# Kernel tuning notes

Measured on AMD Instinct MI355X. Metric: run time of the kernel, lower is better.

## Reference

```python
import jax, jax.numpy as jnp
import numpy as np
from jax import lax

RATE = 2
KSIZE = 3
FUSE_K = 3
PAD = 1
SCALE = 10.0
ESCAPE_NAN = 1e-4
DN = ('NCHW', 'OIHW', 'NCHW')


def _patches(x, k, s, p):
    # x: [C,H,W] -> [L, C, k, k]  (matches torch pad + unfold(2).unfold(3) + permute)
    C = x.shape[0]
    pt = lax.conv_general_dilated_patches(
        x[None], (k, k), (s, s), [(p, p), (p, p)], dimension_numbers=DN)[0]
    oh, ow = pt.shape[1], pt.shape[2]
    # feature dim ordered (c, kh, kw)
    return pt.reshape(C, k, k, oh * ow).transpose(3, 0, 1, 2)


def setup_inputs() -> dict:
    key = jax.random.key(0)
    k1, k2 = jax.random.split(key)
    f = jax.random.normal(k1, (2, 128, 128, 128), dtype=jnp.float32)
    b = jax.random.normal(k2, (2, 128, 128, 128), dtype=jnp.float32)
    mask = jnp.zeros((1, 1, 128, 128), dtype=jnp.float32)
    return {"f": f, "b": b, "mask": mask}


def reference(f, b, mask):
    B, C, H, W = f.shape
    kernel = 2 * RATE  # 4
    # raw background patches (values for conv_transpose), per sample: [L, C, 4, 4]
    raw_w = jax.vmap(lambda bi: _patches(bi, kernel, RATE, PAD))(b)
    # nearest downsample by rate (torch nearest with scale 1/2 == strided slice)
    fd = f[:, :, ::RATE, ::RATE]
    bd = b[:, :, ::RATE, ::RATE]
    md = mask[:, :, ::RATE, ::RATE]
    fh, fw = fd.shape[2], fd.shape[3]
    bh, bw = bd.shape[2], bd.shape[3]
    L = bh * bw
    # matching (key) patches: [B, L, C, 3, 3]
    w = jax.vmap(lambda bi: _patches(bi, KSIZE, 1, PAD))(bd)
    # mask patches -> mm[l] = 1 where patch mean == 0 (valid background)
    m = _patches(md[0], KSIZE, 1, PAD)           # [L, 1, 3, 3]
    mm = (jnp.mean(m, axis=(1, 2, 3)) == 0.0).astype(f.dtype)[:, None, None]  # [L,1,1]

    fuse_w = jnp.eye(FUSE_K, dtype=f.dtype).reshape(1, 1, FUSE_K, FUSE_K)

    def fuse_conv(y):
        return lax.conv_general_dilated(y, fuse_w, (1, 1), [(1, 1), (1, 1)],
                                        dimension_numbers=DN)

    def one(xi, wi, rwi):
        # xi: [C,fh,fw], wi: [L,C,3,3], rwi: [L,C,4,4]
        norm = jnp.sqrt(jnp.sum(wi * wi, axis=(1, 2, 3), keepdims=True))
        wn = wi / jnp.maximum(norm, ESCAPE_NAN)
        # correlation scores (QK^T analogue): [1, L, fh, fw]
        yi = lax.conv_general_dilated(xi[None], wn, (1, 1), [(1, 1), (1, 1)],
                                      dimension_numbers=DN)
        # diagonal fuse convs, exactly mirroring the torch view/permute sequence
        yi = yi.reshape(1, 1, fh * fw, bh * bw)
        yi = fuse_conv(yi)
        yi = yi.reshape(fh, fw, bh, bw).transpose(1, 0, 3, 2).reshape(1, 1, fh * fw, bh * bw)
        yi = fuse_conv(yi)
        yi = yi.reshape(fw, fh, bw, bh).transpose(1, 0, 3, 2)  # [fh, fw, bh, bw]
        # faithful to the torch .view (plain contiguous reshape, no transpose)
        yi = yi.reshape(bh * bw, fh, fw)
        yi = yi * mm
        yi = jax.nn.softmax(yi * SCALE, axis=0) * mm
        # conv_transpose2d(yi, rwi, stride=rate, padding=1) / 4
        wt = jnp.flip(rwi, axis=(2, 3)).transpose(1, 0, 2, 3)  # [C, L, 4, 4]
        p = kernel - 1 - PAD  # 2
        out = lax.conv_general_dilated(yi[None], wt, (1, 1), [(p, p), (p, p)],
                                       lhs_dilation=(RATE, RATE),
                                       dimension_numbers=DN) / 4.0
        return out[0]  # [C, H, W]

    y = jax.vmap(one)(fd, w, raw_w)  # [B, C, H, W]
    return y
```

## Files before the change

### kernel.cpp

```cpp
#include <hip/hip_runtime.h>

#define CC 128
#define HH 128
#define WW 128
#define DH 64
#define DW 64
#define LTOT 4096
#define K0S 384
#define K2 2048
#define GK 4096
#define GKH 2048
#define SCALE_F 10.0f
#define IMG ((size_t)CC * HH * WW)
#define PSTR 4104

typedef __attribute__((ext_vector_type(8))) short short8;
typedef __attribute__((ext_vector_type(4))) float f32x4;

struct Prep4 { const float* src[4]; unsigned short* dst[4]; float* ssq[4]; int lo[4]; };
struct PtrN2 { const float* ssq[2]; float* invn[2]; float* mmv[2]; };
struct PtrR2 { const float* src[2]; unsigned short* dst[2]; };

__device__ __forceinline__ unsigned short f2bf(float x) {
    union { float f; unsigned u; } v; v.f = x;
    unsigned r = v.u + 0x7fffu + ((v.u >> 16) & 1u);
    return (unsigned short)(r >> 16);
}
__device__ __forceinline__ float bf2f(unsigned short b) {
    union { unsigned u; float f; } v; v.u = ((unsigned)b) << 16;
    return v.f;
}

__device__ __forceinline__ f32x4 ld4u(const float* p) {
    f32x4 r; __builtin_memcpy(&r, p, 16); return r;
}

#define GLDS16(g, l) __builtin_amdgcn_global_load_lds( \
    (const __attribute__((address_space(1))) void*)(g), \
    (__attribute__((address_space(3))) void*)(l), 16, 0, 0)

__global__ __launch_bounds__(128) void split_ds_kernel(Prep4 P) {
    __shared__ float partial[2];
    int z = blockIdx.z;
    const float* __restrict__ src = P.src[z];
    unsigned short* __restrict__ dst = P.dst[z];
    int lo_in_seg1 = P.lo[z];
    int n = blockIdx.x;
    int c = threadIdx.x;
    int ny = n >> 6, nx = n & 63;
    float v = src[((size_t)c * HH + 2 * ny) * WW + 2 * nx];
    unsigned short hi = f2bf(v);
    unsigned short lo = f2bf(v - bf2f(hi));
    unsigned short* drow = dst + (size_t)n * K0S;
    drow[c]       = hi;
    drow[128 + c] = lo_in_seg1 ? lo : hi;
    drow[256 + c] = lo_in_seg1 ? hi : lo;

    float* ssq = P.ssq[z];
    if (ssq) {
        float s2 = v * v;
#pragma unroll
        for (int o = 32; o; o >>= 1) s2 += __shfl_xor(s2, o);
        if ((threadIdx.x & 63) == 0) partial[threadIdx.x >> 6] = s2;
        __syncthreads();
        if (threadIdx.x == 0) ssq[n] = partial[0] + partial[1];
    }
}

__global__ __launch_bounds__(256) void im2col_rawt_kernel(PtrR2 P) {
    int z = blockIdx.z;
    const float* __restrict__ src = P.src[z];
    unsigned short* __restrict__ dst = P.dst[z];
    int idx = blockIdx.x * 256 + threadIdx.x;
    int p = idx & (LTOT - 1);
    int m = idx >> 12;
    int px = p & 63, py = p >> 6;
    int ke = m & 3, kd = (m >> 2) & 3, c = m >> 4;
    int yy = 2 * py - 1 + kd, xx = 2 * px - 1 + ke;
    float v = 0.f;
    if (yy >= 0 && yy < HH && xx >= 0 && xx < WW)
        v = src[((size_t)c * HH + yy) * WW + xx];
    dst[idx] = f2bf(v);
}

__global__ void norm_mm_kernel(PtrN2 P, const float* __restrict__ mask) {
    int z = blockIdx.z;
    const float* __restrict__ ssq = P.ssq[z];
    float* __restrict__ inv_norm = P.invn[z];
    float* __restrict__ mmv = P.mmv[z];
    int p = blockIdx.x * blockDim.x + threadIdx.x;
    int px = p & 63, py = p >> 6;
    float s = 0.f, ms = 0.f;
    for (int di = -1; di <= 1; ++di)
        for (int dj = -1; dj <= 1; ++dj) {
            int y = py + di, x = px + dj;
            if (y >= 0 && y < DH && x >= 0 && x < DW) {
                s += ssq[y * 64 + x];
                ms += mask[(size_t)(2 * y) * WW + 2 * x];
            }
        }
    float n = sqrtf(s);
    if (n < 1e-4f) n = 1e-4f;
    inv_norm[p] = 1.f / n;
    mmv[p] = (ms == 0.f) ? 1.f : 0.f;
}

__global__ __launch_bounds__(256) void gemm_mfma(
    const unsigned short* __restrict__ Aop, const unsigned short* __restrict__ Bop,
    float* __restrict__ C, int M, int N, int K)
{
    __shared__ short As[128 * 64];
    __shared__ short Bs[128 * 64];
    int tid = threadIdx.x;
    int wave = tid >> 6, lane = tid & 63;
    int wm = (wave >> 1) * 64;
    int wn = (wave & 1) * 64;
    int bm = blockIdx.y * 128, bn = blockIdx.x * 128;

    int rowS = wave * 32;
    int lrow8 = lane >> 3;
    int gchunk = ((lane & 7) ^ lrow8) * 8;

    f32x4 acc[4][4] = {};

    int quad = lane >> 4;
    int r16 = lane & 15;
    int pc0 = ((quad)     ^ (r16 & 7)) * 8;
    int pc1 = ((4 + quad) ^ (r16 & 7)) * 8;

    const unsigned short* ap0 = Aop + (size_t)(bm + rowS +  0 + lrow8) * K + gchunk;
    const unsigned short* ap1 = Aop + (size_t)(bm + rowS +  8 + lrow8) * K + gchunk;
    const unsigned short* ap2 = Aop + (size_t)(bm + rowS + 16 + lrow8) * K + gchunk;
    const unsigned short* ap3 = Aop + (size_t)(bm + rowS + 24 + lrow8) * K + gchunk;
    const unsigned short* bp0 = Bop + (size_t)(bn + rowS +  0 + lrow8) * K + gchunk;
    const unsigned short* bp1 = Bop + (size_t)(bn + rowS +  8 + lrow8) * K + gchunk;
    const unsigned short* bp2 = Bop + (size_t)(bn + rowS + 16 + lrow8) * K + gchunk;
    const unsigned short* bp3 = Bop + (size_t)(bn + rowS + 24 + lrow8) * K + gchunk;
    short* lA = As + rowS * 64;
    short* lB = Bs + rowS * 64;

    for (int k0 = 0; k0 < K; k0 += 64) {
        GLDS16(ap0, lA);            GLDS16(ap1, lA + 8 * 64);
        GLDS16(ap2, lA + 16 * 64);  GLDS16(ap3, lA + 24 * 64);
        GLDS16(bp0, lB);            GLDS16(bp1, lB + 8 * 64);
        GLDS16(bp2, lB + 16 * 64);  GLDS16(bp3, lB + 24 * 64);
        ap0 += 64; ap1 += 64; ap2 += 64; ap3 += 64;
        bp0 += 64; bp1 += 64; bp2 += 64; bp3 += 64;
        __syncthreads();

        short8 a0[4], b0[4], a1[4], b1[4];
#pragma unroll
        for (int i = 0; i < 4; ++i) {
            a0[i] = *(const short8*)&As[(wm + i * 16 + r16) * 64 + pc0];
            b0[i] = *(const short8*)&Bs[(wn + i * 16 + r16) * 64 + pc0];
            a1[i] = *(const short8*)&As[(wm + i * 16 + r16) * 64 + pc1];
            b1[i] = *(const short8*)&Bs[(wn + i * 16 + r16) * 64 + pc1];
        }
#pragma unroll
        for (int i = 0; i < 4; ++i)
#pragma unroll
            for (int j = 0; j < 4; ++j) {
                acc[i][j] = __builtin_amdgcn_mfma_f32_16x16x32_bf16(a0[i], b0[j], acc[i][j], 0, 0, 0);
                acc[i][j] = __builtin_amdgcn_mfma_f32_16x16x32_bf16(a1[i], b1[j], acc[i][j], 0, 0, 0);
            }
        __syncthreads();
    }

    int col = lane & 15, rq = (lane >> 4) * 4;
#pragma unroll
    for (int i = 0; i < 4; ++i) {
#pragma unroll
        for (int r = 0; r < 4; ++r) {
            int m = bm + wm + i * 16 + rq + r;
#pragma unroll
            for (int j = 0; j < 4; ++j)
                C[(size_t)m * N + bn + wn + j * 16 + col] = acc[i][j][r];
        }
    }
}

__global__ __launch_bounds__(512, 2) void gemm_k2(
    const unsigned short* __restrict__ Aop, const unsigned short* __restrict__ Bop,
    float* __restrict__ Cpart)
{
    constexpr int NT = 32;
    constexpr int BUFS = 512 * 64;
    __shared__ short lds[2 * BUFS];
    int tid = threadIdx.x;
    int wave = tid >> 6, lane = tid & 63;
    int wm = (wave >> 2) * 128;
    int wn = (wave & 3) * 64;
    int bm = blockIdx.y * 256, bn = blockIdx.x * 256;
    int ks = blockIdx.z;
    int lrow8 = lane >> 3;
    int gchunk = ((lane & 7) ^ lrow8) * 8;
    int r16 = lane & 15, quad = lane >> 4;
    int pc0 = ((quad)     ^ (r16 & 7)) * 8;
    int pc1 = ((4 + quad) ^ (r16 & 7)) * 8;

    const size_t ko = (size_t)ks * GKH + gchunk;
    const unsigned short* ap0 = Aop + (size_t)(bm + wave * 32 +  0 + lrow8) * GK + ko;
    const unsigned short* ap1 = Aop + (size_t)(bm + wave * 32 +  8 + lrow8) * GK + ko;
    const unsigned short* ap2 = Aop + (size_t)(bm + wave * 32 + 16 + lrow8) * GK + ko;
    const unsigned short* ap3 = Aop + (size_t)(bm + wave * 32 + 24 + lrow8) * GK + ko;
    const unsigned short* bp0 = Bop + (size_t)(bn + wave * 32 +  0 + lrow8) * GK + ko;
    const unsigned short* bp1 = Bop + (size_t)(bn + wave * 32 +  8 + lrow8) * GK + ko;
    const unsigned short* bp2 = Bop + (size_t)(bn + wave * 32 + 16 + lrow8) * GK + ko;
    const unsigned short* bp3 = Bop + (size_t)(bn + wave * 32 + 24 + lrow8) * GK + ko;

    f32x4 acc[8][4] = {};

#define STAGE2(s) do { \
    short* la = lds + (s) * BUFS + (wave * 32) * 64; \
    short* lb = lds + (s) * BUFS + 256 * 64 + (wave * 32) * 64; \
    GLDS16(ap0, la);            GLDS16(ap1, la + 8 * 64); \
    GLDS16(ap2, la + 16 * 64);  GLDS16(ap3, la + 24 * 64); \
    GLDS16(bp0, lb);            GLDS16(bp1, lb + 8 * 64); \
    GLDS16(bp2, lb + 16 * 64);  GLDS16(bp3, lb + 24 * 64); \
    ap0 += 64; ap1 += 64; ap2 += 64; ap3 += 64; \
    bp0 += 64; bp1 += 64; bp2 += 64; bp3 += 64; } while (0)

    STAGE2(0); STAGE2(1);
    asm volatile("s_waitcnt vmcnt(8)" ::: "memory");
    __builtin_amdgcn_s_barrier();
    asm volatile("" ::: "memory");

    int buf = 0;
#pragma unroll 1
    for (int T = 0; T < NT; ++T) {
        const short* Ab = lds + buf * BUFS;
        const short* Bb = Ab + 256 * 64;
        short8 a0[8], a1[8], b0[4], b1[4];
#pragma unroll
        for (int j = 0; j < 4; ++j) {
            b0[j] = *(const short8*)&Bb[(wn + j * 16 + r16) * 64 + pc0];
            b1[j] = *(const short8*)&Bb[(wn + j * 16 + r16) * 64 + pc1];
        }
        a0[0] = *(const short8*)&Ab[(wm + r16) * 64 + pc0];
        a1[0] = *(const short8*)&Ab[(wm + r16) * 64 + pc1];
#pragma unroll
        for (int i = 0; i < 8; ++i) {
            if (i < 7) {
                a0[i + 1] = *(const short8*)&Ab[(wm + (i + 1) * 16 + r16) * 64 + pc0];
                a1[i + 1] = *(const short8*)&Ab[(wm + (i + 1) * 16 + r16) * 64 + pc1];
                asm volatile("s_waitcnt lgkmcnt(2)" ::: "memory");
            } else {
                asm volatile("s_waitcnt lgkmcnt(0)" ::: "memory");
            }
            __builtin_amdgcn_sched_barrier(0);
            __builtin_amdgcn_s_setprio(1);
#pragma unroll
            for (int j = 0; j < 4; ++j) {
                acc[i][j] = __builtin_amdgcn_mfma_f32_16x16x32_bf16(a0[i], b0[j], acc[i][j], 0, 0, 0);
                acc[i][j] = __builtin_amdgcn_mfma_f32_16x16x32_bf16(a1[i], b1[j], acc[i][j], 0, 0, 0);
            }
            __builtin_amdgcn_s_setprio(0);
        }
        asm volatile("s_waitcnt vmcnt(0)" ::: "memory");
        __builtin_amdgcn_s_barrier();
        asm volatile("" ::: "memory");
        if (T + 2 < NT) STAGE2(buf);
        buf ^= 1;
    }
#undef STAGE2

    float* Cout = Cpart + (size_t)ks * K2 * LTOT;
    int col = lane & 15, rq = (lane >> 4) * 4;
#pragma unroll
    for (int i = 0; i < 8; ++i) {
#pragma unroll
        for (int r = 0; r < 4; ++r) {
            int m = bm + wm + i * 16 + rq + r;
#pragma unroll
            for (int j = 0; j < 4; ++j)
                Cout[(size_t)m * LTOT + bn + wn + j * 16 + col] = acc[i][j][r];
        }
    }
}

__global__ __launch_bounds__(256) void stencil_norm_kernel(
    const float* __restrict__ C, const float* __restrict__ invn,
    float* __restrict__ Sg)
{
    int blk = blockIdx.x;
    int q = ((blk & 7) << 9) | (blk >> 3);
    int t = threadIdx.x;
    int qy = q >> 6, qx = q & 63;
    int chunk = t >> 2;
    int lanebase = (t & 3) << 4;
    int p0 = t << 4;

    f32x4 acc[4];
#pragma unroll
    for (int g = 0; g < 4; ++g) { acc[g][0] = acc[g][1] = acc[g][2] = acc[g][3] = 0.f; }

#pragma unroll
    for (int du = -1; du <= 1; ++du) {
        if (qy + du < 0 || qy + du > 63) continue;
        if (chunk + du < 0 || chunk + du > 63) continue;
#pragma unroll
        for (int dv = -1; dv <= 1; ++dv) {
            if (qx + dv < 0 || qx + dv > 63) continue;
            const float* rowp = C + (size_t)(q + 64 * du + dv) * LTOT + 64 * du + dv + p0;
#pragma unroll
            for (int g = 0; g < 4; ++g) {
                f32x4 lv = ld4u(rowp + 4 * g);
                if (dv == -1 && g == 0 && lanebase == 0)  lv[0] = 0.f;
                if (dv ==  1 && g == 3 && lanebase == 48) lv[3] = 0.f;
                acc[g] += lv;
            }
        }
    }
    float* orow = Sg + (size_t)q * PSTR;
#pragma unroll
    for (int g = 0; g < 4; ++g) {
        f32x4 iv = *(const f32x4*)(invn + p0 + 4 * g);
        *(f32x4*)(orow + p0 + 4 * g) = acc[g] * iv;
    }
    if (t == 0) { orow[-4] = orow[-3] = orow[-2] = orow[-1] = 0.f; }
    else if (t == 1) { orow[4096] = orow[4097] = orow[4098] = orow[4099] = 0.f; }
    if (q == 0) {
        float* gr = Sg - 4 - PSTR;
        for (int k = t; k < PSTR; k += 256) gr[k] = 0.f;
    }
    if (q == 4095) {
        float* gr = Sg - 4 + (size_t)4096 * PSTR;
        for (int k = t; k < PSTR; k += 256) gr[k] = 0.f;
    }
}

__global__ __launch_bounds__(256) void fused_conv_softmax_kernel(
    const float* __restrict__ Sg, const float* __restrict__ mmv,
    unsigned short* __restrict__ S16)
{
    __shared__ float redmax[4];
    __shared__ float redsum[4];
    int blk = blockIdx.x;
    int q = ((blk & 7) << 9) | (blk >> 3);
    int t = threadIdx.x;
    int lane = t & 63, wid = t >> 6;
    int chunk = t >> 2;
    int lanebase = (t & 3) << 4;
    int c0 = t << 4;

    int rbase = ((q & 63) << 6) | (q >> 6);

    f32x4 sacc[4];
#pragma unroll
    for (int g = 0; g < 4; ++g) { sacc[g][0] = sacc[g][1] = sacc[g][2] = sacc[g][3] = 0.f; }

#pragma unroll
    for (int j = 0; j < 3; ++j) {
        int r2 = rbase + (j - 1);
        if (r2 < 0 || r2 >= LTOT) continue;
        int rr = ((r2 & 63) << 6) | (r2 >> 6);
        int cj = chunk + (j - 1);
        int ccb;
        if (cj < 0)       ccb = 4031 + lanebase;
        else if (cj > 63) ccb = lanebase + 1;
        else              ccb = (cj << 6) + lanebase;
        const float* pr = Sg + (size_t)rr * PSTR + ccb;
#pragma unroll
        for (int g = 0; g < 4; ++g) {
            const float* pg = pr + 4 * g;
            f32x4 lm = ld4u(pg - (PSTR + 1));
            f32x4 l0 = ld4u(pg);
            f32x4 lp = ld4u(pg + (PSTR + 1));
            f32x4 tj = lm + l0 + lp;
            if (j == 0 && g == 0 && t == 0)   tj[0] = 0.f;
            if (j == 2 && g == 3 && t == 255) tj[3] = 0.f;
            sacc[g] += tj;
        }
    }

    float v[16];
#pragma unroll
    for (int g = 0; g < 4; ++g) {
        f32x4 m4 = *(const f32x4*)(mmv + c0 + 4 * g);
#pragma unroll
        for (int e = 0; e < 4; ++e)
            v[4 * g + e] = sacc[g][e] * m4[e] * SCALE_F;
    }
#pragma unroll
    for (int k = 0; k < 16; ++k) asm volatile("" : "+v"(v[k]));

    float mx = v[0];
#pragma unroll
    for (int i = 1; i < 16; ++i) mx = fmaxf(mx, v[i]);
#pragma unroll
    for (int o = 32; o; o >>= 1) mx = fmaxf(mx, __shfl_xor(mx, o));
    if (lane == 0) redmax[wid] = mx;
    __syncthreads();
    float gmx = fmaxf(fmaxf(redmax[0], redmax[1]), fmaxf(redmax[2], redmax[3]));

    float s = 0.f;
#pragma unroll
    for (int i = 0; i < 16; ++i) {
        v[i] = __expf(v[i] - gmx);
        s += v[i];
    }
#pragma unroll
    for (int o = 32; o; o >>= 1) s += __shfl_xor(s, o);
    if (lane == 0) redsum[wid] = s;
    __syncthreads();
    float inv = 1.f / (redsum[0] + redsum[1] + redsum[2] + redsum[3]);

    unsigned short* orow = S16 + (size_t)q * LTOT + c0;
    short8 h0, h1;
#pragma unroll
    for (int e = 0; e < 8; ++e) {
        h0[e] = (short)f2bf(v[e]     * inv * mmv[c0 + e]);
        h1[e] = (short)f2bf(v[8 + e] * inv * mmv[c0 + 8 + e]);
    }
    *(short8*)orow = h0;
    *(short8*)(orow + 8) = h1;
}

__global__ void output_kernel(const float* __restrict__ C2t, float* __restrict__ out) {
    const float* __restrict__ P1 = C2t + (size_t)K2 * LTOT;
    int idx = blockIdx.x * blockDim.x + threadIdx.x;
    int x = idx & 127;
    int y = (idx >> 7) & 127;
    int c = idx >> 14;
    int oylo = max(0, (y - 1) >> 1), oyhi = min(63, (y + 1) >> 1);
    int oxlo = max(0, (x - 1) >> 1), oxhi = min(63, (x + 1) >> 1);
    float s = 0.f;
    for (int oy = oylo; oy <= oyhi; ++oy)
        for (int ox = oxlo; ox <= oxhi; ++ox) {
            int kd = y - 2 * oy + 1;
            int ke = x - 2 * ox + 1;
            size_t off = (size_t)(c * 16 + kd * 4 + ke) * LTOT + oy * 64 + ox;
            s += C2t[off] + P1[off];
        }
    out[idx] = s * 0.25f;
}

extern "C" void kernel_launch(void* const* d_in, const int* in_sizes, int n_in,
                              void* d_out, int out_size, void* d_ws, size_t ws_size,
                              hipStream_t stream) {
    (void)in_sizes; (void)n_in; (void)out_size; (void)ws_size;
    const float* f    = (const float*)d_in[0];
    const float* b    = (const float*)d_in[1];
    const float* mask = (const float*)d_in[2];
    float* out = (float*)d_out;

    const size_t SZ_MAT  = (size_t)LTOT * LTOT * 4;
    const size_t SZ_SPAD = (size_t)PSTR * 4098 * 4;
    const size_t SZ_WR   = (size_t)K2 * LTOT * 2;
    const size_t SZ_SP   = (size_t)LTOT * K0S * 2;
    const size_t SZ_V    = (size_t)LTOT * 4;

    auto pad = [](size_t n) { return (n + 255) & ~(size_t)255; };
    char* p = (char*)d_ws;
    auto take = [&](size_t n) -> void* { void* r = (void*)p; p += pad(n); return r; };

    take(256);
    float* Buf1 = (float*)take(SZ_MAT);
    float* Spad = (float*)take(SZ_SPAD);
    unsigned short* W = (unsigned short*)take(SZ_WR);
    unsigned short* Bsp0 = (unsigned short*)take(SZ_SP);
    unsigned short* Fsp0 = (unsigned short*)take(SZ_SP);
    unsigned short* Bsp1 = (unsigned short*)take(SZ_SP);
    unsigned short* Fsp1 = (unsigned short*)take(SZ_SP);
    float* ssq0 = (float*)take(SZ_V);  float* ssq1 = (float*)take(SZ_V);
    float* invn0 = (float*)take(SZ_V); float* invn1 = (float*)take(SZ_V);
    float* mmv0 = (float*)take(SZ_V);  float* mmv1 = (float*)take(SZ_V);

    const float* f0 = f,  *b0 = b;
    const float* f1 = f + IMG, *b1 = b + IMG;

    float* Sg = Spad + PSTR + 4;
    unsigned short* S16 = (unsigned short*)Buf1;
    float* C2t = Spad;

    Prep4 P{{b0, f0, b1, f1}, {Bsp0, Fsp0, Bsp1, Fsp1},
            {ssq0, nullptr, ssq1, nullptr}, {1, 0, 1, 0}};
    split_ds_kernel<<<dim3(LTOT, 1, 4), 128, 0, stream>>>(P);
    PtrN2 nm{{ssq0, ssq1}, {invn0, invn1}, {mmv0, mmv1}};
    norm_mm_kernel<<<dim3(16, 1, 2), 256, 0, stream>>>(nm, mask);

    for (int bi = 0; bi < 2; ++bi) {
        const unsigned short* Fsp = bi ? Fsp1 : Fsp0;
        const unsigned short* Bsp = bi ? Bsp1 : Bsp0;
        const float* invn = bi ? invn1 : invn0;
        const float* mmv  = bi ? mmv1 : mmv0;

        PtrR2 rw{{bi ? b1 : b0, nullptr}, {W, nullptr}};
        im2col_rawt_kernel<<<dim3((size_t)K2 * LTOT / 256, 1, 1), 256, 0, stream>>>(rw);

        gemm_mfma<<<dim3(32, 32), 256, 0, stream>>>(Fsp, Bsp, Buf1, LTOT, LTOT, K0S);

        stencil_norm_kernel<<<LTOT, 256, 0, stream>>>(Buf1, invn, Sg);

        fused_conv_softmax_kernel<<<LTOT, 256, 0, stream>>>(Sg, mmv, S16);

        gemm_k2<<<dim3(LTOT / 256, K2 / 256, 2), 512, 0, stream>>>(W, S16, C2t);

        output_kernel<<<CC * HH * WW / 256, 256, 0, stream>>>(C2t, out + (size_t)bi * IMG);
    }
}
```

Before: 512.4 us.

## Restructure split-K GEMM main loop into four barrier-separated quadrant phases

```diff
diff --git a/kernel.cpp b/kernel.cpp
--- a/kernel.cpp
+++ b/kernel.cpp
@@ -184,8 +184,7 @@
     float* __restrict__ Cpart)
 {
     constexpr int NT = 32;
-    constexpr int BUFS = 512 * 64;
-    __shared__ short lds[2 * BUFS];
+    __shared__ short lds[65536];
     int tid = threadIdx.x;
     int wave = tid >> 6, lane = tid & 63;
     int wm = (wave >> 2) * 128;
@@ -197,72 +196,135 @@
     int r16 = lane & 15, quad = lane >> 4;
     int pc0 = ((quad)     ^ (r16 & 7)) * 8;
     int pc1 = ((4 + quad) ^ (r16 & 7)) * 8;
+    int ha = wave >> 2;
+    int hb = (wave & 3) >> 1;
 
     const size_t ko = (size_t)ks * GKH + gchunk;
-    const unsigned short* ap0 = Aop + (size_t)(bm + wave * 32 +  0 + lrow8) * GK + ko;
-    const unsigned short* ap1 = Aop + (size_t)(bm + wave * 32 +  8 + lrow8) * GK + ko;
-    const unsigned short* ap2 = Aop + (size_t)(bm + wave * 32 + 16 + lrow8) * GK + ko;
-    const unsigned short* ap3 = Aop + (size_t)(bm + wave * 32 + 24 + lrow8) * GK + ko;
-    const unsigned short* bp0 = Bop + (size_t)(bn + wave * 32 +  0 + lrow8) * GK + ko;
-    const unsigned short* bp1 = Bop + (size_t)(bn + wave * 32 +  8 + lrow8) * GK + ko;
-    const unsigned short* bp2 = Bop + (size_t)(bn + wave * 32 + 16 + lrow8) * GK + ko;
-    const unsigned short* bp3 = Bop + (size_t)(bn + wave * 32 + 24 + lrow8) * GK + ko;
+    const unsigned short* aS00 = Aop + (size_t)(bm +       wave * 16 +     lrow8) * GK + ko;
+    const unsigned short* aS01 = Aop + (size_t)(bm +       wave * 16 + 8 + lrow8) * GK + ko;
+    const unsigned short* aS10 = Aop + (size_t)(bm + 128 + wave * 16 +     lrow8) * GK + ko;
+    const unsigned short* aS11 = Aop + (size_t)(bm + 128 + wave * 16 + 8 + lrow8) * GK + ko;
+    const unsigned short* bS00 = Bop + (size_t)(bn +       wave * 16 +     lrow8) * GK + ko;
+    const unsigned short* bS01 = Bop + (size_t)(bn +       wave * 16 + 8 + lrow8) * GK + ko;
+    const unsigned short* bS10 = Bop + (size_t)(bn + 128 + wave * 16 +     lrow8) * GK + ko;
+    const unsigned short* bS11 = Bop + (size_t)(bn + 128 + wave * 16 + 8 + lrow8) * GK + ko;
+
+    const short* ArdH = lds + ha * 8192;
+    const short* BrdH = lds + 32768 + hb * 8192 + (wn & 64) * 64;
+    short* AstH = lds + (wave * 16) * 64;
+    short* BstH = lds + 32768 + (wave * 16) * 64;
 
     f32x4 acc[8][4] = {};
-
-#define STAGE2(s) do { \
-    short* la = lds + (s) * BUFS + (wave * 32) * 64; \
-    short* lb = lds + (s) * BUFS + 256 * 64 + (wave * 32) * 64; \
-    GLDS16(ap0, la);            GLDS16(ap1, la + 8 * 64); \
-    GLDS16(ap2, la + 16 * 64);  GLDS16(ap3, la + 24 * 64); \
-    GLDS16(bp0, lb);            GLDS16(bp1, lb + 8 * 64); \
-    GLDS16(bp2, lb + 16 * 64);  GLDS16(bp3, lb + 24 * 64); \
-    ap0 += 64; ap1 += 64; ap2 += 64; ap3 += 64; \
-    bp0 += 64; bp1 += 64; bp2 += 64; bp3 += 64; } while (0)
-
-    STAGE2(0); STAGE2(1);
+    short8 aa0[4], aa1[4], b0[4], b1[4];
+
+#define STAGE_B2(d) do { short* p = BstH + (d) * 16384; \
+    GLDS16(bS00, p);        GLDS16(bS01, p + 512); \
+    GLDS16(bS10, p + 8192); GLDS16(bS11, p + 8192 + 512); \
+    bS00 += 64; bS01 += 64; bS10 += 64; bS11 += 64; } while (0)
+#define STAGE_A2(d) do { short* p = AstH + (d) * 16384; \
+    GLDS16(aS00, p);        GLDS16(aS01, p + 512); \
+    GLDS16(aS10, p + 8192); GLDS16(aS11, p + 8192 + 512); \
+    aS00 += 64; aS01 += 64; aS10 += 64; aS11 += 64; } while (0)
+#define BARRIER do { __builtin_amdgcn_s_barrier(); asm volatile("" ::: "memory"); } while (0)
+#define WAIT_LGKM0 do { asm volatile("s_waitcnt lgkmcnt(0)" ::: "memory"); \
+    __builtin_amdgcn_sched_barrier(0); } while (0)
+#define MFMA_BF16 __builtin_amdgcn_mfma_f32_16x16x32_bf16
+
+    STAGE_B2(0); STAGE_A2(0); STAGE_B2(1); STAGE_A2(1);
     asm volatile("s_waitcnt vmcnt(8)" ::: "memory");
-    __builtin_amdgcn_s_barrier();
-    asm volatile("" ::: "memory");
-
-    int buf = 0;
+    BARRIER;
+    {
+        const short* Bb = BrdH;
+        b0[0] = *(const short8*)&Bb[(r16) * 64 + pc0];
+        b1[0] = *(const short8*)&Bb[(r16) * 64 + pc1];
+        b0[1] = *(const short8*)&Bb[(16 + r16) * 64 + pc0];
+        b1[1] = *(const short8*)&Bb[(16 + r16) * 64 + pc1];
+    }
+
 #pragma unroll 1
-    for (int T = 0; T < NT; ++T) {
-        const short* Ab = lds + buf * BUFS;
-        const short* Bb = Ab + 256 * 64;
-        short8 a0[8], a1[8], b0[4], b1[4];
-#pragma unroll
-        for (int j = 0; j < 4; ++j) {
-            b0[j] = *(const short8*)&Bb[(wn + j * 16 + r16) * 64 + pc0];
-            b1[j] = *(const short8*)&Bb[(wn + j * 16 + r16) * 64 + pc1];
-        }
-        a0[0] = *(const short8*)&Ab[(wm + r16) * 64 + pc0];
-        a1[0] = *(const short8*)&Ab[(wm + r16) * 64 + pc1];
-#pragma unroll
-        for (int i = 0; i < 8; ++i) {
-            if (i < 7) {
-                a0[i + 1] = *(const short8*)&Ab[(wm + (i + 1) * 16 + r16) * 64 + pc0];
-                a1[i + 1] = *(const short8*)&Ab[(wm + (i + 1) * 16 + r16) * 64 + pc1];
-                asm volatile("s_waitcnt lgkmcnt(2)" ::: "memory");
-            } else {
-                asm volatile("s_waitcnt lgkmcnt(0)" ::: "memory");
-            }
-            __builtin_amdgcn_sched_barrier(0);
-            __builtin_amdgcn_s_setprio(1);
-#pragma unroll
-            for (int j = 0; j < 4; ++j) {
-                acc[i][j] = __builtin_amdgcn_mfma_f32_16x16x32_bf16(a0[i], b0[j], acc[i][j], 0, 0, 0);
-                acc[i][j] = __builtin_amdgcn_mfma_f32_16x16x32_bf16(a1[i], b1[j], acc[i][j], 0, 0, 0);
-            }
-            __builtin_amdgcn_s_setprio(0);
-        }
-        asm volatile("s_waitcnt vmcnt(0)" ::: "memory");
-        __builtin_amdgcn_s_barrier();
-        asm volatile("" ::: "memory");
-        if (T + 2 < NT) STAGE2(buf);
-        buf ^= 1;
-    }
-#undef STAGE2
+    for (int t = 0; t < NT; ++t) {
+        int d = t & 1;
+        const short* Ab = ArdH + d * 16384;
+        const short* Bb = BrdH + d * 16384;
+
+#pragma unroll
+        for (int ii = 0; ii < 4; ++ii) {
+            aa0[ii] = *(const short8*)&Ab[(ii * 16 + r16) * 64 + pc0];
+            aa1[ii] = *(const short8*)&Ab[(ii * 16 + r16) * 64 + pc1];
+        }
+        BARRIER; WAIT_LGKM0;
+        __builtin_amdgcn_s_setprio(1);
+#pragma unroll
+        for (int ii = 0; ii < 4; ++ii)
+#pragma unroll
+            for (int j = 0; j < 2; ++j) {
+                acc[ii][j] = MFMA_BF16(aa0[ii], b0[j], acc[ii][j], 0, 0, 0);
+                acc[ii][j] = MFMA_BF16(aa1[ii], b1[j], acc[ii][j], 0, 0, 0);
+            }
+        __builtin_amdgcn_s_setprio(0);
+        BARRIER;
+
+        b0[2] = *(const short8*)&Bb[(32 + r16) * 64 + pc0];
+        b1[2] = *(const short8*)&Bb[(32 + r16) * 64 + pc1];
+        b0[3] = *(const short8*)&Bb[(48 + r16) * 64 + pc0];
+        b1[3] = *(const short8*)&Bb[(48 + r16) * 64 + pc1];
+        BARRIER; WAIT_LGKM0;
+        __builtin_amdgcn_s_setprio(1);
+#pragma unroll
+        for (int ii = 0; ii < 4; ++ii)
+#pragma unroll
+            for (int j = 2; j < 4; ++j) {
+                acc[ii][j] = MFMA_BF16(aa0[ii], b0[j], acc[ii][j], 0, 0, 0);
+                acc[ii][j] = MFMA_BF16(aa1[ii], b1[j], acc[ii][j], 0, 0, 0);
+            }
+        __builtin_amdgcn_s_setprio(0);
+        BARRIER;
+
+#pragma unroll
+        for (int ii = 0; ii < 4; ++ii) {
+            aa0[ii] = *(const short8*)&Ab[(64 + ii * 16 + r16) * 64 + pc0];
+            aa1[ii] = *(const short8*)&Ab[(64 + ii * 16 + r16) * 64 + pc1];
+        }
+        if (t + 2 < NT) STAGE_B2(d);
+        BARRIER; WAIT_LGKM0;
+        __builtin_amdgcn_s_setprio(1);
+#pragma unroll
+        for (int ii = 0; ii < 4; ++ii)
+#pragma unroll
+            for (int j = 0; j < 2; ++j) {
+                acc[4 + ii][j] = MFMA_BF16(aa0[ii], b0[j], acc[4 + ii][j], 0, 0, 0);
+                acc[4 + ii][j] = MFMA_BF16(aa1[ii], b1[j], acc[4 + ii][j], 0, 0, 0);
+            }
+        __builtin_amdgcn_s_setprio(0);
+        BARRIER;
+
+        if (t + 2 < NT) { asm volatile("s_waitcnt vmcnt(4)" ::: "memory"); }
+        else            { asm volatile("s_waitcnt vmcnt(0)" ::: "memory"); }
+        if (t + 1 < NT) {
+            const short* Bn = BrdH + (d ^ 1) * 16384;
+            b0[0] = *(const short8*)&Bn[(r16) * 64 + pc0];
+            b1[0] = *(const short8*)&Bn[(r16) * 64 + pc1];
+            b0[1] = *(const short8*)&Bn[(16 + r16) * 64 + pc0];
+            b1[1] = *(const short8*)&Bn[(16 + r16) * 64 + pc1];
+        }
+        if (t + 2 < NT) STAGE_A2(d);
+        BARRIER; WAIT_LGKM0;
+        __builtin_amdgcn_s_setprio(1);
+#pragma unroll
+        for (int ii = 0; ii < 4; ++ii)
+#pragma unroll
+            for (int j = 2; j < 4; ++j) {
+                acc[4 + ii][j] = MFMA_BF16(aa0[ii], b0[j], acc[4 + ii][j], 0, 0, 0);
+                acc[4 + ii][j] = MFMA_BF16(aa1[ii], b1[j], acc[4 + ii][j], 0, 0, 0);
+            }
+        __builtin_amdgcn_s_setprio(0);
+        BARRIER;
+    }
+#undef STAGE_B2
+#undef STAGE_A2
+#undef BARRIER
+#undef WAIT_LGKM0
+#undef MFMA_BF16
 
     float* Cout = Cpart + (size_t)ks * K2 * LTOT;
     int col = lane & 15, rq = (lane >> 4) * 4;
```

Result: slower. 524.7 us (+2.4%).
